# Kernel tuning notes

Hardware: AMD Instinct MI355X
Metric: run time of the kernel (lower is better)

## Reference

```python
import jax, jax.numpy as jnp
import numpy as np

G, B, DEG, BATCH = 4000, 8, 32, 128  # genes, per-gene layersize, off-diag blocks/gene, batch


def setup_inputs() -> dict:
    key = jax.random.key(0)
    rng = np.random.default_rng(0)
    # block structure: DEG off-diagonal PPI blocks per gene + reflexive diagonal
    src = np.repeat(np.arange(G, dtype=np.int32), DEG)
    off = 1 + rng.integers(0, G - 1, size=G * DEG)          # never 0 -> off-diagonal
    dst = ((src.astype(np.int64) + off) % G).astype(np.int32)
    diag = np.arange(G, dtype=np.int32)
    block_in = jnp.asarray(np.concatenate([src, diag]))      # [N] = [G*DEG + G]
    block_out = jnp.asarray(np.concatenate([dst, diag]))     # [N]
    n_blocks = G * DEG + G
    k1, k2 = jax.random.split(key)
    x = jax.random.normal(k1, (BATCH, G * B), dtype=jnp.float32)
    w = jax.random.normal(k2, (n_blocks, B, B), dtype=jnp.float32) * 0.05
    return {"x": x, "w": w, "block_in": block_in, "block_out": block_out}


def reference(x, w, block_in, block_out):
    batch, d = x.shape
    n_blocks, b, _ = w.shape
    g = d // b
    xb = x.reshape(batch, g, b)
    xin = xb[:, block_in, :]                        # [batch, N, b] irregular gather
    contrib = jnp.einsum('bni,nio->nbo', xin, w)    # [N, batch, b] tiny per-block GEMMs
    out = jax.ops.segment_sum(contrib, block_out, num_segments=g)  # [g, batch, b] scatter-add
    out = jnp.transpose(out, (1, 0, 2)).reshape(batch, d)
    # activation_function is identity (default lambda x: x); residual=True
    return out + x
```

## Files before the change

kernel.cpp:

```cpp
#include <hip/hip_runtime.h>
#include <hip/hip_bf16.h>

#define G      4000
#define DEG    32
#define BATCH  128
#define D      32000
#define NBLK   132000
#define ZBLK   NBLK
#define CAP    96
#define SCAP   112

typedef __attribute__((ext_vector_type(8))) short bf16x8;
typedef __attribute__((ext_vector_type(4))) float f32x4;

__device__ inline unsigned bf16rne(float f) {
    unsigned u = __float_as_uint(f);
    return (u + 0x7fffu + ((u >> 16) & 1u)) >> 16;
}

__global__ void zero_cnt_kernel(int* cnt) {
    int i = blockIdx.x * 256 + threadIdx.x;
    if (i < G) cnt[i] = 0;
}

#define NB_BUILD 516
#define NB_TR    1000
#define NB_W     2063

__global__ __launch_bounds__(256) void prep_kernel(const float* __restrict__ x,
                                                   const float* __restrict__ w,
                                                   const int* __restrict__ block_in,
                                                   const int* __restrict__ block_out,
                                                   int* __restrict__ cnt,
                                                   int2* __restrict__ pairs,
                                                   unsigned short* __restrict__ xgb,
                                                   unsigned short* __restrict__ wtb) {
    __shared__ float shmem[64 * 68];
    const int bid = blockIdx.x;
    const int t   = threadIdx.x;

    if (bid < NB_BUILD) {
        int n = bid * 256 + t;
        if (n < NBLK) {
            int dst = block_out[n];
            int src = block_in[n];
            int pos = atomicAdd(&cnt[dst], 1);
            if (pos < CAP) pairs[dst * CAP + pos] = make_int2(n, src);
        }
    } else if (bid < NB_BUILD + NB_TR) {
        int id = bid - NB_BUILD;
        int c0 = (id % 250) * 128;
        int b0 = (id / 250) * 32;
        int half = (b0 >= 64) ? 1 : 0;
        int lr0  = b0 & 63;
#pragma unroll
        for (int it = 0; it < 4; ++it) {
            int l  = it * 1024 + t * 4;
            int br = l >> 7;
            int c  = l & 127;
            float4 v = *(const float4*)(x + (size_t)(b0 + br) * D + c0 + c);
            *(float4*)&shmem[br * 132 + c] = v;
        }
        __syncthreads();
#pragma unroll
        for (int it = 0; it < 2; ++it) {
            int idx = it * 256 + t;
            int gl  = idx >> 5;
            int bl  = idx & 31;
            float4 v0 = *(const float4*)&shmem[bl * 132 + gl * 8];
            float4 v1 = *(const float4*)&shmem[bl * 132 + gl * 8 + 4];
            uint4 p;
            p.x = bf16rne(v0.x) | (bf16rne(v0.y) << 16);
            p.y = bf16rne(v0.z) | (bf16rne(v0.w) << 16);
            p.z = bf16rne(v1.x) | (bf16rne(v1.y) << 16);
            p.w = bf16rne(v1.z) | (bf16rne(v1.w) << 16);
            int gidx = (c0 >> 3) + gl;
            size_t base = (((size_t)half * G + gidx) * 64 + lr0 + bl) * 8;
            *(uint4*)(xgb + base) = p;
        }
    } else {
        int    id       = bid - (NB_BUILD + NB_TR);
        size_t base_blk = (size_t)id * 64;
        const float* wb = w + base_blk * 64;
#pragma unroll
        for (int j = 0; j < 4; ++j) {
            int pos  = j * 1024 + t * 4;
            int nl   = pos >> 6;
            int rest = pos & 63;
            float4 v;
            if (base_blk + nl < NBLK) v = *(const float4*)(wb + pos);
            else                      v = make_float4(0.f, 0.f, 0.f, 0.f);
            *(float4*)&shmem[nl * 68 + rest] = v;
        }
        __syncthreads();
#pragma unroll
        for (int j = 0; j < 2; ++j) {
            int p  = j * 256 + t;
            int nl = p >> 3;
            int o  = p & 7;
            size_t nglob = base_blk + nl;
            if (nglob <= NBLK) {
                const float* r = &shmem[nl * 68 + o];
                uint4 q;
                q.x = bf16rne(r[0])  | (bf16rne(r[8])  << 16);
                q.y = bf16rne(r[16]) | (bf16rne(r[24]) << 16);
                q.z = bf16rne(r[32]) | (bf16rne(r[40]) << 16);
                q.w = bf16rne(r[48]) | (bf16rne(r[56]) << 16);
                *(uint4*)(wtb + nglob * 64 + o * 8) = q;
            }
        }
    }
}

__global__ __launch_bounds__(128) void compute_kernel(const float* __restrict__ x,
                                                      const unsigned short* __restrict__ xgb,
                                                      const unsigned short* __restrict__ wtb,
                                                      const int2* __restrict__ pairs,
                                                      const int* __restrict__ cnt,
                                                      float* __restrict__ out) {
    const int blk  = blockIdx.x;
    const int xcd8 = blk & 7;
    const int half = xcd8 >> 2;
    const int g    = (blk >> 3) * 4 + (blk & 3);
    const int t    = threadIdx.x;
    const int wave = t >> 6;
    const int lane = t & 63;
    const int quad = lane >> 4;
    const int lo16 = lane & 15;

    __shared__ int2 se[SCAP];

    int m = cnt[g];
    if (m > CAP) m = CAP;
    if (t < SCAP) {
        int2 e = (t < m) ? pairs[(size_t)g * CAP + t] : make_int2(ZBLK, 0);
        se[t] = e;
    }
    __syncthreads();

    const int ob    = lo16 & 7;
    const int bboff = ob * 8;
    const int mt0   = wave * 32 + lo16;
    const int a0off = mt0 * 8;
    const int a1off = a0off + 128;
    const size_t hbase = (size_t)half * G;

    f32x4 acc0 = {0.f, 0.f, 0.f, 0.f};
    f32x4 acc1 = {0.f, 0.f, 0.f, 0.f};

#define LOADAB(k0, A0, A1, BB)                                            \
    do {                                                                  \
        int2 e_ = se[(k0) + quad];                                        \
        const unsigned short* xb_ = xgb + ((hbase + e_.y) << 9);          \
        A0 = *(const uint4*)(xb_ + a0off);                                \
        A1 = *(const uint4*)(xb_ + a1off);                                \
        BB = *(const uint4*)(wtb + (((size_t)e_.x) << 6) + bboff);        \
    } while (0)

#define CONS(A0, A1, BB)                                                  \
    do {                                                                  \
        acc0 = __builtin_amdgcn_mfma_f32_16x16x32_bf16(                   \
            __builtin_bit_cast(bf16x8, A0), __builtin_bit_cast(bf16x8, BB), acc0, 0, 0, 0); \
        acc1 = __builtin_amdgcn_mfma_f32_16x16x32_bf16(                   \
            __builtin_bit_cast(bf16x8, A1), __builtin_bit_cast(bf16x8, BB), acc1, 0, 0, 0); \
    } while (0)

    uint4 Pa0, Pa1, Pb, Qa0, Qa1, Qb, Ra0, Ra1, Rb, Sa0, Sa1, Sb;

    LOADAB(0,  Pa0, Pa1, Pb);
    LOADAB(4,  Qa0, Qa1, Qb);
    LOADAB(8,  Ra0, Ra1, Rb);
    LOADAB(12, Sa0, Sa1, Sb);

    for (int k0 = 0; k0 < m; k0 += 16) {
        CONS(Pa0, Pa1, Pb);
        LOADAB(k0 + 16, Pa0, Pa1, Pb);
        CONS(Qa0, Qa1, Qb);
        LOADAB(k0 + 20, Qa0, Qa1, Qb);
        CONS(Ra0, Ra1, Rb);
        LOADAB(k0 + 24, Ra0, Ra1, Rb);
        CONS(Sa0, Sa1, Sb);
        LOADAB(k0 + 28, Sa0, Sa1, Sb);
    }

    if (lo16 < 8) {
        const int col = g * 8 + lo16;
#pragma unroll
        for (int r = 0; r < 4; ++r) {
            int row0 = half * 64 + wave * 32 + quad * 4 + r;
            int row1 = row0 + 16;
            out[(size_t)row0 * D + col] = acc0[r] + x[(size_t)row0 * D + col];
            out[(size_t)row1 * D + col] = acc1[r] + x[(size_t)row1 * D + col];
        }
    }
#undef LOADAB
#undef CONS
}

extern "C" void kernel_launch(void* const* d_in, const int* in_sizes, int n_in,
                              void* d_out, int out_size, void* d_ws, size_t ws_size,
                              hipStream_t stream) {
    const float* x         = (const float*)d_in[0];
    const float* w         = (const float*)d_in[1];
    const int*   block_in  = (const int*)d_in[2];
    const int*   block_out = (const int*)d_in[3];
    float*       out       = (float*)d_out;

    char* ws = (char*)d_ws;
    int*            cnt   = (int*)ws;
    int2*           pairs = (int2*)(ws + 16384);
    unsigned short* xgb   = (unsigned short*)(ws + 3088384);
    unsigned short* wtb   = (unsigned short*)(ws + 11280384);

    zero_cnt_kernel<<<16, 256, 0, stream>>>(cnt);
    prep_kernel<<<NB_BUILD + NB_TR + NB_W, 256, 0, stream>>>(x, w, block_in, block_out,
                                                             cnt, pairs, xgb, wtb);
    compute_kernel<<<G * 2, 128, 0, stream>>>(x, xgb, wtb, pairs, cnt, out);
}
```

Baseline: 141.6 us.

## Fuse zero, prep and compute into one cooperative persistent kernel with grid syncs

Replaces the three kernel launches with a single cooperative kernel of 1024 persistent blocks. The blocks zero the counters, loop over the prep units, then loop over compute tiles with two 128-thread compute units per 256-thread block, using grid-wide syncs between phases. The aim is to cut launch overhead and inter-kernel gaps. In exchange it adds grid-barrier cost, fixes the grid size with possibly lower occupancy, and keeps the old three-kernel path as a fallback if the cooperative launch fails.

Result: slower. 305.4 us (+115.7%).

```diff
diff --git a/kernel.cpp b/kernel.cpp
--- a/kernel.cpp
+++ b/kernel.cpp
@@ -1,5 +1,8 @@
 #include <hip/hip_runtime.h>
 #include <hip/hip_bf16.h>
+#include <hip/hip_cooperative_groups.h>
+
+namespace cg = cooperative_groups;
 
 #define G      4000
 #define DEG    32
@@ -10,6 +13,12 @@
 #define CAP    96
 #define SCAP   112
 
+#define NB_BUILD 516
+#define NB_TR    1000
+#define NB_W     2063
+#define NB_PREP  (NB_BUILD + NB_TR + NB_W)
+#define GRID_NB  1024
+
 typedef __attribute__((ext_vector_type(8))) short bf16x8;
 typedef __attribute__((ext_vector_type(4))) float f32x4;
 
@@ -18,37 +27,25 @@
     return (u + 0x7fffu + ((u >> 16) & 1u)) >> 16;
 }
 
-__global__ void zero_cnt_kernel(int* cnt) {
-    int i = blockIdx.x * 256 + threadIdx.x;
-    if (i < G) cnt[i] = 0;
-}
-
-#define NB_BUILD 516
-#define NB_TR    1000
-#define NB_W     2063
-
-__global__ __launch_bounds__(256) void prep_kernel(const float* __restrict__ x,
-                                                   const float* __restrict__ w,
-                                                   const int* __restrict__ block_in,
-                                                   const int* __restrict__ block_out,
-                                                   int* __restrict__ cnt,
-                                                   int2* __restrict__ pairs,
-                                                   unsigned short* __restrict__ xgb,
-                                                   unsigned short* __restrict__ wtb) {
-    __shared__ float shmem[64 * 68];
-    const int bid = blockIdx.x;
-    const int t   = threadIdx.x;
-
-    if (bid < NB_BUILD) {
-        int n = bid * 256 + t;
+__device__ __forceinline__ void prep_unit(int u, int t, float* shmem,
+                                          const float* __restrict__ x,
+                                          const float* __restrict__ w,
+                                          const int* __restrict__ block_in,
+                                          const int* __restrict__ block_out,
+                                          int* __restrict__ cnt,
+                                          int2* __restrict__ pairs,
+                                          unsigned short* __restrict__ xgb,
+                                          unsigned short* __restrict__ wtb) {
+    if (u < NB_BUILD) {
+        int n = u * 256 + t;
         if (n < NBLK) {
             int dst = block_out[n];
             int src = block_in[n];
             int pos = atomicAdd(&cnt[dst], 1);
             if (pos < CAP) pairs[dst * CAP + pos] = make_int2(n, src);
         }
-    } else if (bid < NB_BUILD + NB_TR) {
-        int id = bid - NB_BUILD;
+    } else if (u < NB_BUILD + NB_TR) {
+        int id = u - NB_BUILD;
         int c0 = (id % 250) * 128;
         int b0 = (id / 250) * 32;
         int half = (b0 >= 64) ? 1 : 0;
@@ -79,7 +76,7 @@
             *(uint4*)(xgb + base) = p;
         }
     } else {
-        int    id       = bid - (NB_BUILD + NB_TR);
+        int    id       = u - (NB_BUILD + NB_TR);
         size_t base_blk = (size_t)id * 64;
         const float* wb = w + base_blk * 64;
 #pragma unroll
@@ -112,23 +109,20 @@
     }
 }
 
-__global__ __launch_bounds__(128) void compute_kernel(const float* __restrict__ x,
-                                                      const unsigned short* __restrict__ xgb,
-                                                      const unsigned short* __restrict__ wtb,
-                                                      const int2* __restrict__ pairs,
-                                                      const int* __restrict__ cnt,
-                                                      float* __restrict__ out) {
-    const int blk  = blockIdx.x;
-    const int xcd8 = blk & 7;
+__device__ __forceinline__ void compute_unit(int T, int t, int2* se,
+                                             const float* __restrict__ x,
+                                             const unsigned short* __restrict__ xgb,
+                                             const unsigned short* __restrict__ wtb,
+                                             const int2* __restrict__ pairs,
+                                             const int* __restrict__ cnt,
+                                             float* __restrict__ out) {
+    const int xcd8 = T & 7;
     const int half = xcd8 >> 2;
-    const int g    = (blk >> 3) * 4 + (blk & 3);
-    const int t    = threadIdx.x;
+    const int g    = (T >> 3) * 4 + (T & 3);
     const int wave = t >> 6;
     const int lane = t & 63;
     const int quad = lane >> 4;
     const int lo16 = lane & 15;
-
-    __shared__ int2 se[SCAP];
 
     int m = cnt[g];
     if (m > CAP) m = CAP;
@@ -197,6 +191,67 @@
 #undef CONS
 }
 
+__global__ __launch_bounds__(256, 4) void fused_kernel(const float* __restrict__ x,
+                                                       const float* __restrict__ w,
+                                                       const int* __restrict__ block_in,
+                                                       const int* __restrict__ block_out,
+                                                       int* __restrict__ cnt,
+                                                       int2* __restrict__ pairs,
+                                                       unsigned short* __restrict__ xgb,
+                                                       unsigned short* __restrict__ wtb,
+                                                       float* __restrict__ out) {
+    cg::grid_group grid = cg::this_grid();
+    __shared__ float shmem[64 * 68];
+    __shared__ int2  se2[2][SCAP];
+    const int bid = blockIdx.x;
+    const int t   = threadIdx.x;
+
+    int i = bid * 256 + t;
+    if (i < G) cnt[i] = 0;
+    grid.sync();
+
+    for (int u = bid; u < NB_PREP; u += GRID_NB) {
+        prep_unit(u, t, shmem, x, w, block_in, block_out, cnt, pairs, xgb, wtb);
+        __syncthreads();
+    }
+    grid.sync();
+
+    const int s    = t >> 7;
+    const int t128 = t & 127;
+    for (int T = bid * 2 + s; T < G * 2; T += 2 * GRID_NB) {
+        compute_unit(T, t128, se2[s], x, xgb, wtb, pairs, cnt, out);
+        __syncthreads();
+    }
+}
+
+__global__ void zero_cnt_kernel(int* cnt) {
+    int i = blockIdx.x * 256 + threadIdx.x;
+    if (i < G) cnt[i] = 0;
+}
+
+__global__ __launch_bounds__(256) void prep_kernel(const float* __restrict__ x,
+                                                   const float* __restrict__ w,
+                                                   const int* __restrict__ block_in,
+                                                   const int* __restrict__ block_out,
+                                                   int* __restrict__ cnt,
+                                                   int2* __restrict__ pairs,
+                                                   unsigned short* __restrict__ xgb,
+                                                   unsigned short* __restrict__ wtb) {
+    __shared__ float shmem[64 * 68];
+    prep_unit(blockIdx.x, threadIdx.x, shmem, x, w, block_in, block_out,
+              cnt, pairs, xgb, wtb);
+}
+
+__global__ __launch_bounds__(128) void compute_kernel(const float* __restrict__ x,
+                                                      const unsigned short* __restrict__ xgb,
+                                                      const unsigned short* __restrict__ wtb,
+                                                      const int2* __restrict__ pairs,
+                                                      const int* __restrict__ cnt,
+                                                      float* __restrict__ out) {
+    __shared__ int2 se[SCAP];
+    compute_unit(blockIdx.x, threadIdx.x, se, x, xgb, wtb, pairs, cnt, out);
+}
+
 extern "C" void kernel_launch(void* const* d_in, const int* in_sizes, int n_in,
                               void* d_out, int out_size, void* d_ws, size_t ws_size,
                               hipStream_t stream) {
@@ -212,8 +267,16 @@
     unsigned short* xgb   = (unsigned short*)(ws + 3088384);
     unsigned short* wtb   = (unsigned short*)(ws + 11280384);
 
-    zero_cnt_kernel<<<16, 256, 0, stream>>>(cnt);
-    prep_kernel<<<NB_BUILD + NB_TR + NB_W, 256, 0, stream>>>(x, w, block_in, block_out,
-                                                             cnt, pairs, xgb, wtb);
-    compute_kernel<<<G * 2, 128, 0, stream>>>(x, xgb, wtb, pairs, cnt, out);
-}
+    void* args[9] = {(void*)&x, (void*)&w, (void*)&block_in, (void*)&block_out,
+                     (void*)&cnt, (void*)&pairs, (void*)&xgb, (void*)&wtb, (void*)&out};
+    hipError_t err = hipLaunchCooperativeKernel((const void*)fused_kernel,
+                                                dim3(GRID_NB), dim3(256),
+                                                args, 0, stream);
+    if (err != hipSuccess) {
+        (void)hipGetLastError();
+        zero_cnt_kernel<<<16, 256, 0, stream>>>(cnt);
+        prep_kernel<<<NB_PREP, 256, 0, stream>>>(x, w, block_in, block_out,
+                                                 cnt, pairs, xgb, wtb);
+        compute_kernel<<<G * 2, 128, 0, stream>>>(x, xgb, wtb, pairs, cnt, out);
+    }
+}
```
